# Kernel tuning notes

Hardware: AMD Instinct MI355X
Metric: run time of the kernel (lower is better)

The kernel has to match this reference:

```python
import jax, jax.numpy as jnp
import numpy as np

ACTIVE_VOCAB = 8192  # current_size == init_vocab (eval mode, no growth)
EPS = 1e-12


def _l2_normalize(v, axis=-1):
    n = jnp.sqrt(jnp.sum(v * v, axis=axis, keepdims=True))
    return v / jnp.maximum(n, EPS)


def setup_inputs() -> dict:
    key = jax.random.key(0)
    k1, k2 = jax.random.split(key)
    B, T, D, V = 8, 2048, 512, 16384
    x = jax.random.normal(k1, (B, T, D), dtype=jnp.float32)
    codebook = jax.random.normal(k2, (V, D), dtype=jnp.float32) * (D ** -0.5)
    return {"x": x, "codebook": codebook}


def reference(x, codebook):
    B, T, D = x.shape
    x_flat = x.reshape(-1, D)                      # (N, D), N = B*T
    x_norm = _l2_normalize(x_flat)
    cb_active = codebook[:ACTIVE_VOCAB]            # (V, D)
    cb_norm = _l2_normalize(cb_active)
    # cosine similarities, compute-heavy GEMM (N x D x V)
    sims = jnp.einsum("nd,vd->nv", x_norm, cb_norm)
    indices = jnp.argmax(sims, axis=-1)            # (N,)
    max_sims = jnp.max(sims, axis=-1)              # (N,)
    # codebook gather (embedding lookup)
    z_q_flat = cb_active[indices]                  # (N, D)
    z_q = z_q_flat.reshape(B, T, D)
    # straight-through estimator
    z_q_ste = x + jax.lax.stop_gradient(z_q - x)
    # usage entropy over active codes
    N = B * T
    counts = jnp.zeros(ACTIVE_VOCAB, jnp.float32).at[indices].add(1.0)
    probs = counts / (N + 1e-9)
    usage_entropy = -jnp.sum(jnp.where(probs > 0, probs * jnp.log(jnp.maximum(probs, EPS)), 0.0))
    mean_sim = jnp.mean(max_sims)
    return z_q_ste, indices.reshape(B, T), usage_entropy, mean_sim
```

## Files before the change

### kernel.cpp

```cpp
#include <hip/hip_runtime.h>

typedef short bf16x8 __attribute__((ext_vector_type(8)));
typedef float f32x4  __attribute__((ext_vector_type(4)));

#define NROW  16384
#define DD    512
#define VOCAB 8192
#define VS    4
#define VCH   2048
#define BM    256
#define BN    256
#define BK    64
#define NCHUNK 8
#define NKT    8
#define NTILE  64

#define CBBF_W   4194304
#define CANDV_W  6291456
#define CANDI_W  6815744
#define OUT_IDX  ((size_t)NROW * DD)
#define OUT_ENT  (OUT_IDX + NROW)
#define OUT_MEAN (OUT_ENT + 1)

#define WS_CBNORM 0
#define WS_MAXSIM 16384
#define WS_COUNTS 32768
#define WS_CANDV  49152
#define WS_CANDI  311296
#define WS_NEED_BYTES ((size_t)(311296 + 262144) * 4)

#define GLD_LDS(g, l) \
    __builtin_amdgcn_global_load_lds((const __attribute__((address_space(1))) void*)(g), \
                                     (__attribute__((address_space(3))) void*)(l), 16, 0, 0)

#define BAR()   __builtin_amdgcn_s_barrier()
#define LGKM0() asm volatile("s_waitcnt lgkmcnt(0)" ::: "memory")
#define VM4()   asm volatile("s_waitcnt vmcnt(4)" ::: "memory")
#define VM0()   asm volatile("s_waitcnt vmcnt(0)" ::: "memory")

__device__ __forceinline__ ushort f2bf(float f) {
    unsigned u = __float_as_uint(f);
    return (ushort)((u + 0x7fffu + ((u >> 16) & 1u)) >> 16);
}

__global__ void eq_prep(const float* __restrict__ x, const float* __restrict__ cb,
                        ushort* __restrict__ xbf, ushort* __restrict__ cbbf,
                        float* __restrict__ nrm, int* __restrict__ counts) {
    const int b = blockIdx.x;
    const int tid = threadIdx.x;
    if (b < 4096) {
        size_t i = ((size_t)b * 256 + tid) * 8;
        float4 v0 = *(const float4*)(x + i);
        float4 v1 = *(const float4*)(x + i + 4);
        ushort r[8] = {f2bf(v0.x), f2bf(v0.y), f2bf(v0.z), f2bf(v0.w),
                       f2bf(v1.x), f2bf(v1.y), f2bf(v1.z), f2bf(v1.w)};
        *(uint4*)(xbf + i) = *(const uint4*)r;
        return;
    }
    const int bb = b - 4096;
    if (bb < 32) counts[bb * 256 + tid] = 0;
    const int row = bb * 4 + (tid >> 6);
    const int l = tid & 63;
    const float* p = cb + (size_t)row * DD;
    float4 a = *(const float4*)(p + l * 4);
    float4 bq = *(const float4*)(p + 256 + l * 4);
    float s = a.x * a.x + a.y * a.y + a.z * a.z + a.w * a.w
            + bq.x * bq.x + bq.y * bq.y + bq.z * bq.z + bq.w * bq.w;
#pragma unroll
    for (int off = 32; off > 0; off >>= 1) s += __shfl_xor(s, off, 64);
    float n = fmaxf(sqrtf(s), 1e-12f);
    float rn = 1.0f / n;
    ushort r0[4] = {f2bf(a.x * rn), f2bf(a.y * rn), f2bf(a.z * rn), f2bf(a.w * rn)};
    ushort r1[4] = {f2bf(bq.x * rn), f2bf(bq.y * rn), f2bf(bq.z * rn), f2bf(bq.w * rn)};
    *(uint2*)(cbbf + (size_t)row * DD + l * 4)       = *(const uint2*)r0;
    *(uint2*)(cbbf + (size_t)row * DD + 256 + l * 4) = *(const uint2*)r1;
    if (l == 0) nrm[row] = n;
}

__global__ __launch_bounds__(512, 2) void eq_gemm_topk(
    const ushort* __restrict__ xbf, const ushort* __restrict__ cbbf,
    float* __restrict__ candval, int* __restrict__ candidx) {
    __shared__ __align__(16) char LDS[131072];
    const int tid = threadIdx.x;
    const int lane = tid & 63;
    const int w = tid >> 6;
    const int wm = w >> 2;
    const int wn = w & 3;
    const int c = lane & 15, q = lane >> 4;

    const int bid = blockIdx.x;
    const int j = bid >> 3;
    const int vsplit = j & 3;
    const int xtile  = (bid & 7) * 8 + (j >> 2);
    const int xbase  = xtile * BN;
    const int vsbase = vsplit * VCH;

    const char* gA = (const char*)cbbf + (size_t)vsbase * 1024;
    const char* gB = (const char*)xbf  + (size_t)xbase  * 1024;
    const int thrOff = (w * 8 + (lane >> 3)) * 1024
                     + (((lane & 7) ^ ((lane >> 3) & 7)) << 4);
    const int wbase = w * 1024;
    const int sw0 = (q ^ (c & 7)) << 4;
    const int sw1 = ((4 + q) ^ (c & 7)) << 4;
    const int aoff0 = wm * 16384 + c * 128 + sw0;
    const int aoff1 = wm * 16384 + c * 128 + sw1;
    const int bbase = 65536 + (wn >> 1) * 16384 + ((wn & 1) * 64 + c) * 128;
    const int boff0 = bbase + sw0;
    const int boff1 = bbase + sw1;

#define STAGE_A(lin2, h) do { int _l = (lin2); if (_l < NTILE) { \
        const char* _s = gA + ((_l >> 3) * 262144 + (h) * 131072 + (_l & 7) * 128) + thrOff; \
        char* _d = (char*)LDS + ((_l & 1) * 32768 + (h) * 16384 + wbase); \
        GLD_LDS(_s, _d); GLD_LDS(_s + 65536, _d + 8192); } } while (0)
#define STAGE_B(lin2, h) do { int _l = (lin2); if (_l < NTILE) { \
        const char* _s = gB + ((h) * 131072 + (_l & 7) * 128) + thrOff; \
        char* _d = (char*)LDS + (65536 + (_l & 1) * 32768 + (h) * 16384 + wbase); \
        GLD_LDS(_s, _d); GLD_LDS(_s + 65536, _d + 8192); } } while (0)

    int t1k[4], t2k[4];
#pragma unroll
    for (int nj = 0; nj < 4; ++nj) { t1k[nj] = 0x80000000; t2k[nj] = 0x80000000; }

    f32x4 acc[8][4];

    STAGE_A(0, 0); STAGE_A(0, 1);
    STAGE_B(0, 0); STAGE_B(0, 1);
    STAGE_A(1, 0); STAGE_A(1, 1);
    VM4(); BAR();

    for (int lin = 0; lin < NTILE; ++lin) {
        const int set = (lin & 1) * 32768;
        if ((lin & 7) == 0) {
#pragma unroll
            for (int mi = 0; mi < 8; ++mi)
#pragma unroll
                for (int nj = 0; nj < 4; ++nj) acc[mi][nj] = (f32x4){0.f, 0.f, 0.f, 0.f};
        }
        bf16x8 af[8], bf0, bf1;
#pragma unroll
        for (int mi = 0; mi < 8; ++mi)
            af[mi] = *(const bf16x8*)(LDS + set + aoff0 + mi * 2048);
        bf0 = *(const bf16x8*)(LDS + set + boff0);
        bf1 = *(const bf16x8*)(LDS + set + boff0 + 2048);
        STAGE_B(lin + 1, 0);
        BAR(); LGKM0();
        __builtin_amdgcn_s_setprio(1);
#pragma unroll
        for (int mi = 0; mi < 8; ++mi) {
            acc[mi][0] = __builtin_amdgcn_mfma_f32_16x16x32_bf16(af[mi], bf0, acc[mi][0], 0, 0, 0);
            acc[mi][1] = __builtin_amdgcn_mfma_f32_16x16x32_bf16(af[mi], bf1, acc[mi][1], 0, 0, 0);
        }
        __builtin_amdgcn_s_setprio(0);
        BAR();
        bf0 = *(const bf16x8*)(LDS + set + boff0 + 4096);
        bf1 = *(const bf16x8*)(LDS + set + boff0 + 6144);
        STAGE_B(lin + 1, 1);
        BAR(); LGKM0();
        __builtin_amdgcn_s_setprio(1);
#pragma unroll
        for (int mi = 0; mi < 8; ++mi) {
            acc[mi][2] = __builtin_amdgcn_mfma_f32_16x16x32_bf16(af[mi], bf0, acc[mi][2], 0, 0, 0);
            acc[mi][3] = __builtin_amdgcn_mfma_f32_16x16x32_bf16(af[mi], bf1, acc[mi][3], 0, 0, 0);
        }
        __builtin_amdgcn_s_setprio(0);
        BAR();
#pragma unroll
        for (int mi = 0; mi < 8; ++mi)
            af[mi] = *(const bf16x8*)(LDS + set + aoff1 + mi * 2048);
        bf0 = *(const bf16x8*)(LDS + set + boff1);
        bf1 = *(const bf16x8*)(LDS + set + boff1 + 2048);
        BAR(); LGKM0();
        __builtin_amdgcn_s_setprio(1);
#pragma unroll
        for (int mi = 0; mi < 8; ++mi) {
            acc[mi][0] = __builtin_amdgcn_mfma_f32_16x16x32_bf16(af[mi], bf0, acc[mi][0], 0, 0, 0);
            acc[mi][1] = __builtin_amdgcn_mfma_f32_16x16x32_bf16(af[mi], bf1, acc[mi][1], 0, 0, 0);
        }
        __builtin_amdgcn_s_setprio(0);
        BAR();
        bf0 = *(const bf16x8*)(LDS + set + boff1 + 4096);
        bf1 = *(const bf16x8*)(LDS + set + boff1 + 6144);
        STAGE_A(lin + 2, 0);
        STAGE_A(lin + 2, 1);
        if (lin < 62) { VM4(); } else { VM0(); }
        BAR(); LGKM0();
        __builtin_amdgcn_s_setprio(1);
#pragma unroll
        for (int mi = 0; mi < 8; ++mi) {
            acc[mi][2] = __builtin_amdgcn_mfma_f32_16x16x32_bf16(af[mi], bf0, acc[mi][2], 0, 0, 0);
            acc[mi][3] = __builtin_amdgcn_mfma_f32_16x16x32_bf16(af[mi], bf1, acc[mi][3], 0, 0, 0);
        }
        __builtin_amdgcn_s_setprio(0);
        BAR();
        if ((lin & 7) == 7) {
            const int chb = (lin >> 3) << 5;
#pragma unroll
            for (int nj = 0; nj < 4; ++nj)
#pragma unroll
                for (int mi = 0; mi < 8; ++mi)
#pragma unroll
                    for (int r = 0; r < 4; ++r) {
                        int key = (__float_as_int(acc[mi][nj][r]) & (int)0xFFFFFF00)
                                | (chb + mi * 4 + r);
                        int mn = t1k[nj] < key ? t1k[nj] : key;
                        t1k[nj] = t1k[nj] < key ? key : t1k[nj];
                        t2k[nj] = t2k[nj] < mn ? mn : t2k[nj];
                    }
        }
    }
#pragma unroll
    for (int nj = 0; nj < 4; ++nj) {
        int k1 = t1k[nj], k2 = t2k[nj];
        float t1v = __int_as_float(k1 & (int)0xFFFFFF00);
        float t2v = __int_as_float(k2 & (int)0xFFFFFF00);
        int l1 = k1 & 255, l2 = k2 & 255;
        int t1i = vsbase + ((l1 >> 5) << 8) + (wm << 7) + (((l1 >> 2) & 7) << 4) + (q << 2) + (l1 & 3);
        int t2i = vsbase + ((l2 >> 5) << 8) + (wm << 7) + (((l2 >> 2) & 7) << 4) + (q << 2) + (l2 & 3);
#pragma unroll
        for (int off = 16; off <= 32; off <<= 1) {
            float o1v = __shfl_xor(t1v, off, 64); int o1i = __shfl_xor(t1i, off, 64);
            float o2v = __shfl_xor(t2v, off, 64); int o2i = __shfl_xor(t2i, off, 64);
            bool wbest = (t1v > o1v) || (t1v == o1v && t1i < o1i);
            float m1 = wbest ? t1v : o1v;  int m1i = wbest ? t1i : o1i;
            float ca = wbest ? o1v : t1v;  int cai = wbest ? o1i : t1i;
            float cw = wbest ? t2v : o2v;  int cwi = wbest ? t2i : o2i;
            bool s2 = (ca > cw) || (ca == cw && cai < cwi);
            t1v = m1;           t1i = m1i;
            t2v = s2 ? ca : cw; t2i = s2 ? cai : cwi;
        }
        if (q == 0) {
            int list = vsplit * 2 + wm;
            int row = xbase + wn * 64 + nj * 16 + c;
            size_t base = ((size_t)list * NROW + row) * 2;
            candval[base] = t1v; candval[base + 1] = t2v;
            candidx[base] = t1i; candidx[base + 1] = t2i;
        }
    }
#undef STAGE_A
#undef STAGE_B
}

template <bool FUSE_ZQ>
__device__ __forceinline__ void rescore_body(
    const float* __restrict__ x, const float* __restrict__ cb,
    const float* __restrict__ cbnorm,
    const float* __restrict__ candval, const int* __restrict__ candidx,
    float* __restrict__ out, float* __restrict__ maxsim, int* __restrict__ counts) {
    int w = threadIdx.x >> 6, l = threadIdx.x & 63;
    int row = blockIdx.x * 4 + w;

    const float4* X4 = (const float4*)(x + (size_t)row * DD);
    float4 xa = X4[l], xb = X4[l + 64];
    float s2 = xa.x * xa.x + xa.y * xa.y + xa.z * xa.z + xa.w * xa.w
             + xb.x * xb.x + xb.y * xb.y + xb.z * xb.z + xb.w * xb.w;
#pragma unroll
    for (int off = 32; off > 0; off >>= 1) s2 += __shfl_xor(s2, off, 64);
    float xn = fmaxf(sqrtf(s2), 1e-12f);
    double xd[8] = {(double)(xa.x / xn), (double)(xa.y / xn), (double)(xa.z / xn),
                    (double)(xa.w / xn), (double)(xb.x / xn), (double)(xb.y / xn),
                    (double)(xb.z / xn), (double)(xb.w / xn)};

    float cv[16]; int ci[16];
#pragma unroll
    for (int t = 0; t < 16; ++t) {
        size_t b = ((size_t)(t >> 1) * NROW + row) * 2 + (t & 1);
        cv[t] = candval[b]; ci[t] = candidx[b];
    }
    float bv1 = cv[0];
#pragma unroll
    for (int t = 1; t < 16; ++t) bv1 = fmaxf(bv1, cv[t]);
    float margin = 2e-3f * xn;

    double best = -1e300; int bi = 1 << 30;
    for (int t = 0; t < 16; ++t) {
        if (cv[t] >= bv1 - margin) {
            float n = cbnorm[ci[t]];
            const float4* C4 = (const float4*)(cb + (size_t)ci[t] * DD);
            float4 ca = C4[l], cb4 = C4[l + 64];
            double a = xd[0] * (double)(ca.x / n) + xd[1] * (double)(ca.y / n)
                     + xd[2] * (double)(ca.z / n) + xd[3] * (double)(ca.w / n)
                     + xd[4] * (double)(cb4.x / n) + xd[5] * (double)(cb4.y / n)
                     + xd[6] * (double)(cb4.z / n) + xd[7] * (double)(cb4.w / n);
#pragma unroll
            for (int off = 32; off > 0; off >>= 1) a += __shfl_xor(a, off, 64);
            bool better = (a > best) || (a == best && ci[t] < bi);
            best = better ? a : best;
            bi = better ? ci[t] : bi;
        }
    }
    if (l == 0) {
        out[OUT_IDX + row] = (float)bi;
        maxsim[row] = (float)best;
        atomicAdd(counts + bi, 1);
    }
    if (FUSE_ZQ) {
        const float4* src = (const float4*)(cb + (size_t)bi * DD);
        float4* dst = (float4*)(out + (size_t)row * DD);
        dst[l] = src[l];
        dst[l + 64] = src[l + 64];
    }
}

__global__ void eq_rescore(const float* __restrict__ x, const float* __restrict__ cb,
                           const float* __restrict__ cbnorm,
                           const float* __restrict__ candval, const int* __restrict__ candidx,
                           float* __restrict__ out, float* __restrict__ maxsim,
                           int* __restrict__ counts) {
    rescore_body<false>(x, cb, cbnorm, candval, candidx, out, maxsim, counts);
}

__global__ void eq_rescore_fused(const float* __restrict__ x, const float* __restrict__ cb,
                                 const float* __restrict__ cbnorm,
                                 const float* __restrict__ candval, const int* __restrict__ candidx,
                                 float* __restrict__ out, float* __restrict__ maxsim,
                                 int* __restrict__ counts) {
    rescore_body<true>(x, cb, cbnorm, candval, candidx, out, maxsim, counts);
}

__global__ void eq_gather(const float* __restrict__ cb, float* __restrict__ out) {
    int w = threadIdx.x >> 6, l = threadIdx.x & 63;
    int row = blockIdx.x * 4 + w;
    int bi = (int)out[OUT_IDX + row];
    const float4* src = (const float4*)(cb + (size_t)bi * DD);
    float4* dst = (float4*)(out + (size_t)row * DD);
    dst[l] = src[l];
    dst[l + 64] = src[l + 64];
}

__global__ void eq_entropy_mean(const int* __restrict__ counts,
                                const float* __restrict__ maxsim,
                                float* __restrict__ out) {
    __shared__ float red[16];
    int tid = threadIdx.x;
    float s = 0.f;
    for (int b = tid; b < VOCAB; b += 1024) {
        int c = counts[b];
        if (c > 0) {
            float p = (float)c * (1.0f / 16384.0f);
            s += p * logf(p);
        }
    }
#pragma unroll
    for (int off = 32; off > 0; off >>= 1) s += __shfl_down(s, off, 64);
    if ((tid & 63) == 0) red[tid >> 6] = s;
    __syncthreads();
    if (tid == 0) {
        float t = 0.f;
#pragma unroll
        for (int i = 0; i < 16; ++i) t += red[i];
        out[OUT_ENT] = -t;
    }
    __syncthreads();
    float m = 0.f;
    for (int i = tid; i < NROW; i += 1024) m += maxsim[i];
#pragma unroll
    for (int off = 32; off > 0; off >>= 1) m += __shfl_down(m, off, 64);
    if ((tid & 63) == 0) red[tid >> 6] = m;
    __syncthreads();
    if (tid == 0) {
        float t = 0.f;
#pragma unroll
        for (int i = 0; i < 16; ++i) t += red[i];
        out[OUT_MEAN] = t * (1.0f / 16384.0f);
    }
}

extern "C" void kernel_launch(void* const* d_in, const int* in_sizes, int n_in,
                              void* d_out, int out_size, void* d_ws, size_t ws_size,
                              hipStream_t stream) {
    const float* x  = (const float*)d_in[0];
    const float* cb = (const float*)d_in[1];
    float* out = (float*)d_out;
    float* wsf = (float*)d_ws;
    int*   wsi = (int*)d_ws;

    float* cbnorm = wsf + WS_CBNORM;
    float* maxsim = wsf + WS_MAXSIM;
    int*   counts = wsi + WS_COUNTS;

    ushort* xbf   = (ushort*)out;
    ushort* cbbf  = (ushort*)(out + CBBF_W);

    const bool fused = ws_size >= WS_NEED_BYTES;
    float* candv = fused ? (wsf + WS_CANDV) : (out + CANDV_W);
    int*   candi = fused ? (wsi + WS_CANDI) : (int*)(out + CANDI_W);

    eq_prep<<<6144, 256, 0, stream>>>(x, cb, xbf, cbbf, cbnorm, counts);

    eq_gemm_topk<<<256, 512, 0, stream>>>(xbf, cbbf, candv, candi);

    if (fused) {
        eq_rescore_fused<<<NROW / 4, 256, 0, stream>>>(x, cb, cbnorm, candv, candi,
                                                       out, maxsim, counts);
    } else {
        eq_rescore<<<NROW / 4, 256, 0, stream>>>(x, cb, cbnorm, candv, candi,
                                                 out, maxsim, counts);
        eq_gather<<<NROW / 4, 256, 0, stream>>>(cb, out);
    }
    eq_entropy_mean<<<1, 1024, 0, stream>>>(counts, maxsim, out);
}
```

Before: 256.2 us.

## Restructure MFMA phases by M-halves and overlap LDS reads with compute

```diff
diff --git a/kernel.cpp b/kernel.cpp
--- a/kernel.cpp
+++ b/kernel.cpp
@@ -136,62 +136,66 @@
 #pragma unroll
                 for (int nj = 0; nj < 4; ++nj) acc[mi][nj] = (f32x4){0.f, 0.f, 0.f, 0.f};
         }
-        bf16x8 af[8], bf0, bf1;
-#pragma unroll
-        for (int mi = 0; mi < 8; ++mi)
+        bf16x8 af[8], af2[8], bfA[4], bfB[4];
+#pragma unroll
+        for (int mi = 0; mi < 4; ++mi)
             af[mi] = *(const bf16x8*)(LDS + set + aoff0 + mi * 2048);
-        bf0 = *(const bf16x8*)(LDS + set + boff0);
-        bf1 = *(const bf16x8*)(LDS + set + boff0 + 2048);
+#pragma unroll
+        for (int nj = 0; nj < 4; ++nj)
+            bfA[nj] = *(const bf16x8*)(LDS + set + boff0 + nj * 2048);
         STAGE_B(lin + 1, 0);
-        BAR(); LGKM0();
+        BAR();
         __builtin_amdgcn_s_setprio(1);
 #pragma unroll
-        for (int mi = 0; mi < 8; ++mi) {
-            acc[mi][0] = __builtin_amdgcn_mfma_f32_16x16x32_bf16(af[mi], bf0, acc[mi][0], 0, 0, 0);
-            acc[mi][1] = __builtin_amdgcn_mfma_f32_16x16x32_bf16(af[mi], bf1, acc[mi][1], 0, 0, 0);
-        }
+        for (int mi = 0; mi < 4; ++mi)
+#pragma unroll
+            for (int nj = 0; nj < 4; ++nj)
+                acc[mi][nj] = __builtin_amdgcn_mfma_f32_16x16x32_bf16(af[mi], bfA[nj], acc[mi][nj], 0, 0, 0);
         __builtin_amdgcn_s_setprio(0);
         BAR();
-        bf0 = *(const bf16x8*)(LDS + set + boff0 + 4096);
-        bf1 = *(const bf16x8*)(LDS + set + boff0 + 6144);
+#pragma unroll
+        for (int mi = 4; mi < 8; ++mi)
+            af[mi] = *(const bf16x8*)(LDS + set + aoff0 + mi * 2048);
+#pragma unroll
+        for (int mi = 0; mi < 4; ++mi)
+            af2[mi] = *(const bf16x8*)(LDS + set + aoff1 + mi * 2048);
         STAGE_B(lin + 1, 1);
-        BAR(); LGKM0();
+        BAR();
         __builtin_amdgcn_s_setprio(1);
 #pragma unroll
-        for (int mi = 0; mi < 8; ++mi) {
-            acc[mi][2] = __builtin_amdgcn_mfma_f32_16x16x32_bf16(af[mi], bf0, acc[mi][2], 0, 0, 0);
-            acc[mi][3] = __builtin_amdgcn_mfma_f32_16x16x32_bf16(af[mi], bf1, acc[mi][3], 0, 0, 0);
-        }
+        for (int mi = 4; mi < 8; ++mi)
+#pragma unroll
+            for (int nj = 0; nj < 4; ++nj)
+                acc[mi][nj] = __builtin_amdgcn_mfma_f32_16x16x32_bf16(af[mi], bfA[nj], acc[mi][nj], 0, 0, 0);
         __builtin_amdgcn_s_setprio(0);
         BAR();
 #pragma unroll
-        for (int mi = 0; mi < 8; ++mi)
-            af[mi] = *(const bf16x8*)(LDS + set + aoff1 + mi * 2048);
-        bf0 = *(const bf16x8*)(LDS + set + boff1);
-        bf1 = *(const bf16x8*)(LDS + set + boff1 + 2048);
-        BAR(); LGKM0();
+        for (int mi = 4; mi < 8; ++mi)
+            af2[mi] = *(const bf16x8*)(LDS + set + aoff1 + mi * 2048);
+#pragma unroll
+        for (int nj = 0; nj < 4; ++nj)
+            bfB[nj] = *(const bf16x8*)(LDS + set + boff1 + nj * 2048);
+        BAR();
         __builtin_amdgcn_s_setprio(1);
 #pragma unroll
-        for (int mi = 0; mi < 8; ++mi) {
-            acc[mi][0] = __builtin_amdgcn_mfma_f32_16x16x32_bf16(af[mi], bf0, acc[mi][0], 0, 0, 0);
-            acc[mi][1] = __builtin_amdgcn_mfma_f32_16x16x32_bf16(af[mi], bf1, acc[mi][1], 0, 0, 0);
-        }
+        for (int mi = 0; mi < 4; ++mi)
+#pragma unroll
+            for (int nj = 0; nj < 4; ++nj)
+                acc[mi][nj] = __builtin_amdgcn_mfma_f32_16x16x32_bf16(af2[mi], bfB[nj], acc[mi][nj], 0, 0, 0);
         __builtin_amdgcn_s_setprio(0);
-        BAR();
-        bf0 = *(const bf16x8*)(LDS + set + boff1 + 4096);
-        bf1 = *(const bf16x8*)(LDS + set + boff1 + 6144);
+        LGKM0();
+        BAR();
         STAGE_A(lin + 2, 0);
         STAGE_A(lin + 2, 1);
         if (lin < 62) { VM4(); } else { VM0(); }
-        BAR(); LGKM0();
+        BAR();
         __builtin_amdgcn_s_setprio(1);
 #pragma unroll
-        for (int mi = 0; mi < 8; ++mi) {
-            acc[mi][2] = __builtin_amdgcn_mfma_f32_16x16x32_bf16(af[mi], bf0, acc[mi][2], 0, 0, 0);
-            acc[mi][3] = __builtin_amdgcn_mfma_f32_16x16x32_bf16(af[mi], bf1, acc[mi][3], 0, 0, 0);
-        }
+        for (int mi = 4; mi < 8; ++mi)
+#pragma unroll
+            for (int nj = 0; nj < 4; ++nj)
+                acc[mi][nj] = __builtin_amdgcn_mfma_f32_16x16x32_bf16(af2[mi], bfB[nj], acc[mi][nj], 0, 0, 0);
         __builtin_amdgcn_s_setprio(0);
-        BAR();
         if ((lin & 7) == 7) {
             const int chb = (lin >> 3) << 5;
 #pragma unroll
```

Measured after the change: 258.3 us. No clear change (+0.8%).
